# Kernel optimization log

Hardware: AMD Instinct MI355X
Metric: run time of the kernel (lower is better)

Reference implementation:

```python
import jax, jax.numpy as jnp
import numpy as np


def _operators_3_to_2(x2d, A, norm):
    # x2d: [b, d, n, n], A: [b, n, n]. Returns the 20 basis tensors, each [b, d, n, n].
    t = lambda a: a.transpose(0, 1, 3, 2)
    shape = x2d.shape
    op1 = jnp.einsum('bdij,bij,bik->bdjk', x2d, A, A) / norm
    op2 = jnp.einsum('bdij,bij,bjk->bdik', x2d, A, A) / norm
    op3 = jnp.einsum('bdij,bik,bjk->bdij', x2d, A, A) / norm
    op4 = jnp.broadcast_to(jnp.einsum('bdij,bij->bdi', x2d, A)[..., None], shape) / norm
    op5 = jnp.broadcast_to(jnp.einsum('bdij,bij->bdj', x2d, A)[..., None], shape) / norm
    op6 = jnp.einsum('bdij,bik->bdjk', x2d, A) / norm
    # NOTE: source has ops7 = [op6, op6.transpose] (bug: op7 computed but unused) -- replicated faithfully.
    op8 = jnp.einsum('bdij,bik->bdij', x2d, A) / norm
    op9 = jnp.einsum('bdij,bjk->bdij', x2d, A) / norm
    op10 = jnp.broadcast_to(x2d.sum(3, keepdims=True), shape) / norm
    op11 = jnp.broadcast_to(x2d.sum(2, keepdims=True), shape) / norm
    return [op1, t(op1), op2, t(op2), op3,
            op4, t(op4), op5, t(op5),
            op6, t(op6), op6, t(op6),
            op8, op9,
            op10, t(op10), op11, t(op11),
            x2d]


def _forward(x, edge_weight, coeffs1, bias1, coeffs2, bias2, edge_index, batch, n):
    f = x.shape[-1]
    b = x.shape[0] // n
    # to_2d_tensor: [b*n, f] -> [b, 2f, n, n]
    x2 = x.reshape(b, n, f).transpose(0, 2, 1)  # [b, f, n]
    x_2d = jnp.concatenate([
        jnp.broadcast_to(x2[:, :, :, None], (b, f, n, n)),
        jnp.broadcast_to(x2[:, :, None, :], (b, f, n, n)),
    ], axis=1)
    # to_dense_adj: scatter-add edge weights into per-graph dense [b, n, n]
    g = batch[edge_index[0]]
    r = edge_index[0] - g * n
    c = edge_index[1] - g * n
    A = jnp.zeros((b, n, n), x.dtype).at[g, r, c].add(edge_weight)
    norm = jnp.asarray(n, x.dtype)  # normalization=True default
    for li, (coeffs, bias) in enumerate([(coeffs1, bias1), (coeffs2, bias2)]):
        ops_out = jnp.stack(_operators_3_to_2(x_2d, A, norm), axis=2)  # [b, d, 20, n, n]
        x_2d = jnp.einsum('der,bdrij->beij', coeffs, ops_out) + bias
        if li == 0:
            x_2d = jax.nn.sigmoid(x_2d)
    return x_2d.mean(axis=(1, 2, 3))  # [b]


def setup_inputs() -> dict:
    key = jax.random.key(0)
    kx, kg, ks, kd, kw, kc1, kc2 = jax.random.split(key, 7)
    b, n, deg, f, h = 4, 128, 16, 32, 32
    d_in, d_out = 2 * f, 2 * h  # layer doubles channels; hidden layer is d_out -> d_out
    E = b * n * deg
    x = jax.random.normal(kx, (b * n, f), dtype=jnp.float32)
    g = jax.random.randint(kg, (E,), 0, b)
    src = jax.random.randint(ks, (E,), 0, n)
    dst = jax.random.randint(kd, (E,), 0, n)
    edge_index = jnp.stack([g * n + src, g * n + dst]).astype(jnp.int32)
    edge_weight = jax.random.uniform(kw, (E,), dtype=jnp.float32)
    batch = (jnp.arange(b * n) // n).astype(jnp.int32)
    scale1 = np.sqrt(2.0) / (d_in + d_out)
    scale2 = np.sqrt(2.0) / (d_out + d_out)
    coeffs1 = jax.random.normal(kc1, (d_in, d_out, 20), dtype=jnp.float32) * scale1
    coeffs2 = jax.random.normal(kc2, (d_out, d_out, 20), dtype=jnp.float32) * scale2
    bias1 = jnp.zeros((1, d_out, 1, 1), dtype=jnp.float32)
    bias2 = jnp.zeros((1, d_out, 1, 1), dtype=jnp.float32)
    return {"x": x, "edge_weight": edge_weight, "coeffs1": coeffs1, "bias1": bias1,
            "coeffs2": coeffs2, "bias2": bias2, "edge_index": edge_index,
            "batch": batch, "n": n}


def reference(x, edge_weight, coeffs1, bias1, coeffs2, bias2, edge_index, batch, n):
    return _forward(x, edge_weight, coeffs1, bias1, coeffs2, bias2, edge_index, batch, n)
```

## Files before the change

kernel.cpp:

```cpp
#include <hip/hip_runtime.h>
#include <stdint.h>

typedef unsigned short u16;
using short8 = __attribute__((ext_vector_type(8))) short;
using f32x4  = __attribute__((ext_vector_type(4))) float;

#define NB 4
#define NN 128
#define NF 32
#define ND 64

#define OFF_A     0u
#define OFF_ACC   262144u
#define OFF_AAT   262400u
#define OFF_RA    524544u
#define OFF_W     526592u
#define OFF_RM    1116416u
#define OFF_CM    1247488u
#define OFF_RX    1378560u
#define OFF_CX    1509632u
#define OFF_BF    1640960u
#define OFF_ATB   1641472u
#define OFF_WB    1772544u
#define OFF_X2    1936384u
#define OFF_XC    10324992u
#define OFF_CA    10357760u
#define OFF_UA    18713600u
#define OFF_UB    27102208u
#define OFF_UC    35490816u
#define OFF_UD    43879424u
#define OFF_YACC  52268032u

__device__ __forceinline__ float b2f(u16 v){
  union { uint32_t u; float f; } x; x.u = ((uint32_t)v) << 16; return x.f;
}
__device__ __forceinline__ u16 f2b(float f){
  union { uint32_t u; float f2; } x; x.f2 = f;
  uint32_t u = x.u;
  return (u16)((u + 0x7FFFu + ((u >> 16) & 1u)) >> 16);
}

#define MFMA16(a,b,c) __builtin_amdgcn_mfma_f32_16x16x32_bf16((a),(b),(c),0,0,0)

__device__ __constant__ signed char dR1[18] = {0,9,1,10,2,3,4,13,14,19,5,7,15,18,6,8,16,17};
__device__ __constant__ signed char dR2[18] = {-1,11,-1,12,-1,-1,-1,-1,-1,-1,-1,-1,-1,-1,-1,-1,-1,-1};

__global__ void k_setup(const int* __restrict__ ei, const int* __restrict__ bat,
                        const void* __restrict__ ews, float* __restrict__ A, int E,
                        const void* __restrict__ xs, u16* __restrict__ xc,
                        const void* __restrict__ c1s, const void* __restrict__ c2s,
                        const void* __restrict__ b1s, const void* __restrict__ b2s,
                        float* __restrict__ W, u16* __restrict__ Wb,
                        float* __restrict__ bfv)
{
  __shared__ int flg;
  const u16* x16 = (const u16*)xs;
  if (threadIdx.x == 0) flg = 0;
  __syncthreads();
  int hit = 0;
  for (int k = threadIdx.x; k < 1024; k += 256){
    u16 u = x16[k];
    if (((u >> 7) & 0xFF) >= 0x90) hit = 1;
  }
  if (hit) flg = 1;
  __syncthreads();
  const int isf = flg;

  const int bx = blockIdx.x;
  if (bx < 32){
    if (bx == 0 && threadIdx.x < 128){
      int tt = threadIdx.x;
      const void* bsrc = (tt < 64) ? b1s : b2s;
      int idx = tt & 63;
      bfv[tt] = isf ? ((const float*)bsrc)[idx] : b2f(((const u16*)bsrc)[idx]);
    }
    for (int t = bx*256 + threadIdx.x; t < E; t += 32*256){
      int s = ei[t], dnode = ei[E + t];
      int g = bat[s];
      int r = s - g*NN, c = dnode - g*NN;
      float wv = isf ? ((const float*)ews)[t] : b2f(((const u16*)ews)[t]);
      atomicAdd(&A[(g*NN + r)*NN + c], wv);
    }
  } else if (bx < 40){
    int idx8 = ((bx - 32)*256 + threadIdx.x)*8;
    if (!isf){
      *(short8*)(xc + idx8) = *(const short8*)(x16 + idx8);
    } else {
      const float* xfp = (const float*)xs;
      short8 v;
      #pragma unroll
      for (int k = 0; k < 8; k++) v[k] = (short)f2b(xfp[idx8 + k]);
      *(short8*)(xc + idx8) = v;
    }
  } else {
    int gl = (bx - 40)*256 + threadIdx.x;
    if (gl >= 2*1152*64) return;
    int L = gl / (1152*64);
    int rem = gl - L*1152*64;
    int row = rem >> 6, e = rem & 63;
    int slot = row >> 6, d = row & 63;
    const void* cr = L ? c2s : c1s;
    int base = (d*64 + e)*20;
    int i1 = base + dR1[slot];
    float v = isf ? ((const float*)cr)[i1] : b2f(((const u16*)cr)[i1]);
    if (dR2[slot] >= 0){
      int i2 = base + dR2[slot];
      v += isf ? ((const float*)cr)[i2] : b2f(((const u16*)cr)[i2]);
    }
    float scale = (slot == 9) ? 1.0f : (1.0f/128.0f);
    v *= scale;
    W[gl] = v;
    if (slot < 10)
      Wb[(((size_t)L*10 + slot)*64 + e)*64 + d] = f2b(v);
  }
}

__global__ __launch_bounds__(256) void k_prepA(const float* __restrict__ A, float* __restrict__ AAt,
                                               u16* __restrict__ ATb, float* __restrict__ rA,
                                               float* __restrict__ cA){
  const int iq = blockIdx.x, b = blockIdx.y;
  const int t = threadIdx.x;
  if (iq < 32){
    int j = t & 127, ih = t >> 7;
    int i0 = iq*4 + ih, i1 = i0 + 2;
    const float* Ab = A + b*NN*NN;
    float acc0 = 0.f, acc1 = 0.f;
    #pragma unroll 4
    for (int k = 0; k < 128; k += 4){
      float4 aj = *(const float4*)(Ab + j*128 + k);
      float4 a0 = *(const float4*)(Ab + i0*128 + k);
      float4 a1 = *(const float4*)(Ab + i1*128 + k);
      acc0 += a0.x*aj.x + a0.y*aj.y + a0.z*aj.z + a0.w*aj.w;
      acc1 += a1.x*aj.x + a1.y*aj.y + a1.z*aj.z + a1.w*aj.w;
    }
    AAt[(b*NN + i0)*NN + j] = acc0;
    AAt[(b*NN + i1)*NN + j] = acc1;
  } else {
    __shared__ float lds[128][129];
    for (int l = 0; l < 64; l++){
      int idx = l*256 + t;
      lds[idx >> 7][idx & 127] = A[b*16384 + idx];
    }
    __syncthreads();
    for (int l = 0; l < 64; l++){
      int idx = l*256 + t;
      int r = idx >> 7, c = idx & 127;
      ATb[b*16384 + idx] = f2b(lds[c][r]);
    }
    if (t < 128){
      float s = 0.f;
      for (int j = 0; j < 128; j++) s += lds[t][j];
      rA[b*NN + t] = s;
    } else {
      int c = t - 128;
      float s = 0.f;
      for (int j = 0; j < 128; j++) s += lds[j][c];
      cA[b*NN + c] = s;
    }
  }
}

#define SJ32 70
#define SJF  67
#define SXE  34

__global__ __launch_bounds__(256) void k_mixrow(const u16* __restrict__ Xs, const float* __restrict__ A,
    const float* __restrict__ AAt, const float* __restrict__ rA, const float* __restrict__ cA,
    const u16* __restrict__ xc, const u16* __restrict__ Wb,
    u16* __restrict__ Ua, u16* __restrict__ Ub, u16* __restrict__ Uc, u16* __restrict__ Ud,
    float* __restrict__ Yacc,
    float* __restrict__ RM, float* __restrict__ CM,
    float* __restrict__ RX, float* __restrict__ CXv, int first)
{
  const int b = blockIdx.y;
  const int t = threadIdx.x;

  if (blockIdx.x >= 256){
    const int d = blockIdx.x - 256;
    if (first){
      if (t < 128){
        const int i = t;
        if (d < NF){
          float xv = b2f(xc[(b*NN + i)*NF + d]);
          RM[(b*64 + d)*128 + i] = xv * rA[b*NN + i];
          RX[(b*64 + d)*128 + i] = 128.f * xv;
        } else {
          const u16* xcb = xc + b*NN*NF + (d - NF);
          const float* Ar = A + b*16384 + i*128;
          float sm = 0.f, sx = 0.f;
          for (int j = 0; j < 128; j++){
            float xj = b2f(xcb[j*NF]);
            sm += Ar[j]*xj; sx += xj;
          }
          RM[(b*64 + d)*128 + i] = sm;
          RX[(b*64 + d)*128 + i] = sx;
        }
      } else {
        const int j = t - 128;
        if (d < NF){
          const u16* xcb = xc + b*NN*NF + d;
          const float* Ac = A + b*16384 + j;
          float sm = 0.f, sx = 0.f;
          for (int i = 0; i < 128; i++){
            float xi = b2f(xcb[i*NF]);
            sm += Ac[i*128]*xi; sx += xi;
          }
          CM[(b*64 + d)*128 + j] = sm;
          CXv[(b*64 + d)*128 + j] = sx;
        } else {
          float xv = b2f(xc[(b*NN + j)*NF + (d - NF)]);
          CM[(b*64 + d)*128 + j] = xv * cA[b*NN + j];
          CXv[(b*64 + d)*128 + j] = 128.f * xv;
        }
      }
      return;
    }
    const u16* Xd = Xs + ((size_t)(b*ND + d) << 14);
    const float* Ab = A + b*NN*NN;
    float sm = 0.f, sx = 0.f;
    if (t < 128){
      const int i = t;
      #pragma unroll 2
      for (int j8 = 0; j8 < 16; j8++){
        short8 xv = *(const short8*)(Xd + i*128 + j8*8);
        float4 a0 = *(const float4*)(Ab + i*128 + j8*8);
        float4 a1 = *(const float4*)(Ab + i*128 + j8*8 + 4);
        float x0 = b2f((u16)xv[0]), x1 = b2f((u16)xv[1]), x2 = b2f((u16)xv[2]), x3 = b2f((u16)xv[3]);
        float x4 = b2f((u16)xv[4]), x5 = b2f((u16)xv[5]), x6 = b2f((u16)xv[6]), x7 = b2f((u16)xv[7]);
        sx += x0+x1+x2+x3+x4+x5+x6+x7;
        sm += x0*a0.x + x1*a0.y + x2*a0.z + x3*a0.w
            + x4*a1.x + x5*a1.y + x6*a1.z + x7*a1.w;
      }
      RM[(b*64 + d)*128 + i] = sm;
      RX[(b*64 + d)*128 + i] = sx;
    } else {
      const int j = t - 128;
      for (int i = 0; i < 128; i++){
        float xv = b2f(Xd[i*128 + j]);
        sx += xv;
        sm += xv * Ab[i*128 + j];
      }
      CM[(b*64 + d)*128 + j] = sm;
      CXv[(b*64 + d)*128 + j] = sx;
    }
    return;
  }

  const int w = t >> 6, lane = t & 63;
  const int col = lane & 15, quad = lane >> 4;
  const int ij0 = blockIdx.x*64;

  __shared__ uint32_t lsb[4][32*SJ32];
  __shared__ float lsf[64*SJF];

  short8 wa[10][2];
  #pragma unroll
  for (int s = 0; s < 10; s++){
    const u16* wp = Wb + (size_t)((s*64 + w*16 + col)*64 + quad*8);
    wa[s][0] = *(const short8*)wp;
    wa[s][1] = *(const short8*)(wp + 32);
  }
  float a_s[4], t_s[4], rjv[4];
  #pragma unroll
  for (int sj = 0; sj < 4; sj++){
    int ij = ij0 + sj*16 + col;
    a_s[sj] = A[b*16384 + ij];
    t_s[sj] = AAt[b*16384 + ij];
    rjv[sj] = rA[b*128 + (ij & 127)];
  }
  const float riv = rA[b*128 + (ij0 >> 7)];

  uint32_t* ldsX = &lsb[0][0];
  {
    const int ep = t >> 3;
    const int s8 = (t & 7)*8;
    if (first){
      const int i = ij0 >> 7;
      const int j0 = (ij0 & 127) + s8;
      if (ep < 16){
        uint32_t p = *(const uint32_t*)(xc + (b*NN + i)*NF + 2*ep);
        #pragma unroll
        for (int k = 0; k < 8; k++) ldsX[(s8 + k)*SXE + ep] = p;
      } else {
        const int d0 = 2*ep - 32;
        #pragma unroll
        for (int k = 0; k < 8; k++)
          ldsX[(s8 + k)*SXE + ep] = *(const uint32_t*)(xc + (b*NN + j0 + k)*NF + d0);
      }
    } else {
      const u16* xp = Xs + ((size_t)(b*ND + 2*ep) << 14) + ij0 + s8;
      short8 r0 = *(const short8*)xp;
      short8 r1 = *(const short8*)(xp + 16384);
      #pragma unroll
      for (int k = 0; k < 8; k++)
        ldsX[(s8 + k)*SXE + ep] = ((uint32_t)(u16)r0[k]) | (((uint32_t)(u16)r1[k]) << 16);
    }
  }
  __syncthreads();
  short8 xb[4][2];
  #pragma unroll
  for (int sj = 0; sj < 4; sj++){
    #pragma unroll
    for (int h = 0; h < 2; h++){
      const uint32_t* p = &ldsX[(sj*16 + col)*SXE + quad*4 + h*16];
      uint2 u0 = *(const uint2*)p;
      uint2 u1 = *(const uint2*)(p + 2);
      union { uint32_t u[4]; short8 s; } cv;
      cv.u[0] = u0.x; cv.u[1] = u0.y; cv.u[2] = u1.x; cv.u[3] = u1.y;
      xb[sj][h] = cv.s;
    }
  }
  __syncthreads();

  #pragma unroll
  for (int g = 0; g < 5; g++){
    const int s0_tab[5]  = {0, 2, 4, 5, 6};
    const int nsl_tab[5] = {2, 2, 1, 1, 4};
    const int s0 = s0_tab[g], nsl = nsl_tab[g];
    #pragma unroll
    for (int sj = 0; sj < 4; sj++){
      f32x4 acc[4];
      #pragma unroll
      for (int s = 0; s < 4; s++) acc[s] = (f32x4){0.f,0.f,0.f,0.f};
      #pragma unroll
      for (int s = 0; s < 4; s++){
        if (s >= nsl) break;
        acc[s] = MFMA16(wa[s0+s][0], xb[sj][0], acc[s]);
        acc[s] = MFMA16(wa[s0+s][1], xb[sj][1], acc[s]);
      }
      if (g < 4){
        float v[4];
        #pragma unroll
        for (int r = 0; r < 4; r++){
          if (g == 2 || g == 3) v[r] = acc[0][r]*a_s[sj];
          else                  v[r] = acc[0][r]*a_s[sj] + acc[1][r];
        }
        uint32_t p0 = (uint32_t)f2b(v[0]) | ((uint32_t)f2b(v[1]) << 16);
        uint32_t p1 = (uint32_t)f2b(v[2]) | ((uint32_t)f2b(v[3]) << 16);
        int ep = w*8 + quad*2;
        lsb[g][ep*SJ32 + sj*16 + col] = p0;
        lsb[g][(ep + 1)*SJ32 + sj*16 + col] = p1;
      } else {
        #pragma unroll
        for (int r = 0; r < 4; r++){
          float v = acc[0][r]*t_s[sj] + acc[1][r]*riv + acc[2][r]*rjv[sj] + acc[3][r];
          lsf[(w*16 + quad*4 + r)*SJF + sj*16 + col] = v;
        }
      }
    }
  }
  __syncthreads();

  const int eo = t >> 2, seg = t & 3;
  const int ep = eo >> 1, sh = (eo & 1)*16;
  #pragma unroll
  for (int g = 0; g < 4; g++){
    const uint32_t* lp = &lsb[g][ep*SJ32 + seg*16];
    short8 v0, v1;
    #pragma unroll
    for (int k = 0; k < 8; k++){
      v0[k] = (short)((lp[k]   >> sh) & 0xffffu);
      v1[k] = (short)((lp[8+k] >> sh) & 0xffffu);
    }
    u16* U = (g==0)?Ua:(g==1)?Ub:(g==2)?Uc:Ud;
    u16* dst = U + ((size_t)(b*64 + eo) << 14) + ij0 + seg*16;
    *(short8*)dst = v0;
    *(short8*)(dst + 8) = v1;
  }
  {
    const float* fp = &lsf[eo*SJF + seg*16];
    float* dst = Yacc + ((size_t)(b*64 + eo) << 14) + ij0 + seg*16;
    #pragma unroll
    for (int q = 0; q < 4; q++)
      *(float4*)(dst + q*4) = make_float4(fp[q*4], fp[q*4+1], fp[q*4+2], fp[q*4+3]);
  }
}

#define SLT 68
#define SST 136

__global__ __launch_bounds__(512) void k_tne(const u16* __restrict__ ATb,
    const u16* __restrict__ Ua, const u16* __restrict__ Ub,
    const u16* __restrict__ Uc, const u16* __restrict__ Ud,
    const float* __restrict__ Yacc, const float* __restrict__ W,
    const float* __restrict__ RM, const float* __restrict__ CM,
    const float* __restrict__ RX, const float* __restrict__ CXv,
    const float* __restrict__ bias, u16* __restrict__ Xout, float* __restrict__ acc4,
    unsigned int* __restrict__ cnt, const u16* __restrict__ x16, void* __restrict__ outp,
    int last)
{
  const int be = blockIdx.x;
  const int b = be >> 6, e = be & 63;
  const int t = threadIdx.x, wave = t >> 6, lane = t & 63;
  const int col = lane & 15, quad = lane >> 4;
  const int m0 = (wave >> 2)*64;
  const int n0 = (wave & 3)*32;

  __shared__ uint32_t uls[128*SLT];
  __shared__ uint32_t ubl[128*SLT];
  __shared__ float radd[128], cadd[128];
  __shared__ float red[8];
  __shared__ int flg, lastblk;

  if (t == 0){ flg = 0; lastblk = 0; }

  const u16* ua = Ua + ((size_t)be << 14);
  const u16* ub = Ub + ((size_t)be << 14);

  if (t < 128){
    int i = t; float s = 0.f;
    for (int d = 0; d < ND; d++){
      int v = (b*ND + d)*NN + i;
      s += W[(640 + d)*64 + e]*RM[v] + W[(704 + d)*64 + e]*CM[v]
         + W[(768 + d)*64 + e]*RX[v] + W[(832 + d)*64 + e]*CXv[v];
    }
    radd[i] = s;
  } else if (t < 256){
    int j = t - 128; float s = 0.f;
    for (int d = 0; d < ND; d++){
      int v = (b*ND + d)*NN + j;
      s += W[(896 + d)*64 + e]*RM[v] + W[(960 + d)*64 + e]*CM[v]
         + W[(1024 + d)*64 + e]*RX[v] + W[(1088 + d)*64 + e]*CXv[v];
    }
    cadd[j] = s;
  } else if (t < 384){
    const int tt = t - 256;
    const int kp = tt >> 1, p = tt & 1;
    #pragma unroll
    for (int it = 0; it < 8; it++){
      int mo = it*2 + p;
      short8 r0 = *(const short8*)(ua + (2*kp)*128 + mo*8);
      short8 r1 = *(const short8*)(ua + (2*kp + 1)*128 + mo*8);
      #pragma unroll
      for (int x = 0; x < 8; x++)
        uls[(mo*8 + x)*SLT + kp] = ((uint32_t)(u16)r0[x]) | (((uint32_t)(u16)r1[x]) << 16);
    }
  } else {
    const int tt = t - 384;
    const int kp = tt >> 1, p = tt & 1;
    #pragma unroll
    for (int it = 0; it < 8; it++){
      int no = it*2 + p;
      short8 r0 = *(const short8*)(ub + (2*kp)*128 + no*8);
      short8 r1 = *(const short8*)(ub + (2*kp + 1)*128 + no*8);
      #pragma unroll
      for (int x = 0; x < 8; x++)
        ubl[(no*8 + x)*SLT + kp] = ((uint32_t)(u16)r0[x]) | (((uint32_t)(u16)r1[x]) << 16);
    }
  }
  __syncthreads();

  f32x4 acc[4][2];
  #pragma unroll
  for (int mt = 0; mt < 4; mt++)
    #pragma unroll
    for (int nt = 0; nt < 2; nt++)
      acc[mt][nt] = (f32x4){0.f,0.f,0.f,0.f};

  const u16* at = ATb + ((size_t)b << 14);
  short8 at_n[4][2];
  #pragma unroll
  for (int kq = 0; kq < 4; kq++){
    int k0 = kq*32 + quad*8;
    at_n[kq][0] = *(const short8*)(at + (n0 + col)*128 + k0);
    at_n[kq][1] = *(const short8*)(at + (n0 + 16 + col)*128 + k0);
  }

  #pragma unroll
  for (int kq = 0; kq < 4; kq++){
    int kd = kq*16 + quad*4;
    #pragma unroll
    for (int mt = 0; mt < 4; mt++){
      short8 af = *(const short8*)&uls[(m0 + mt*16 + col)*SLT + kd];
      acc[mt][0] = MFMA16(af, at_n[kq][0], acc[mt][0]);
      acc[mt][1] = MFMA16(af, at_n[kq][1], acc[mt][1]);
    }
  }
  #pragma unroll
  for (int kq = 0; kq < 4; kq++){
    int k0 = kq*32 + quad*8, kd = kq*16 + quad*4;
    short8 bf0 = *(const short8*)&ubl[(n0 + col)*SLT + kd];
    short8 bf1 = *(const short8*)&ubl[(n0 + 16 + col)*SLT + kd];
    #pragma unroll
    for (int mt = 0; mt < 4; mt++){
      short8 af = *(const short8*)(at + (m0 + mt*16 + col)*128 + k0);
      acc[mt][0] = MFMA16(af, bf0, acc[mt][0]);
      acc[mt][1] = MFMA16(af, bf1, acc[mt][1]);
    }
  }
  {
    const u16* uc = Uc + ((size_t)be << 14);
    #pragma unroll
    for (int kq = 0; kq < 4; kq++){
      int k0 = kq*32 + quad*8;
      #pragma unroll
      for (int mt = 0; mt < 4; mt++){
        short8 af = *(const short8*)(uc + (m0 + mt*16 + col)*128 + k0);
        acc[mt][0] = MFMA16(af, at_n[kq][0], acc[mt][0]);
        acc[mt][1] = MFMA16(af, at_n[kq][1], acc[mt][1]);
      }
    }
  }
  {
    const u16* ud = Ud + ((size_t)be << 14);
    #pragma unroll
    for (int kq = 0; kq < 4; kq++){
      int k0 = kq*32 + quad*8;
      short8 bf0 = *(const short8*)(ud + (n0 + col)*128 + k0);
      short8 bf1 = *(const short8*)(ud + (n0 + 16 + col)*128 + k0);
      #pragma unroll
      for (int mt = 0; mt < 4; mt++){
        short8 af = *(const short8*)(at + (m0 + mt*16 + col)*128 + k0);
        acc[mt][0] = MFMA16(af, bf0, acc[mt][0]);
        acc[mt][1] = MFMA16(af, bf1, acc[mt][1]);
      }
    }
  }
  __syncthreads();

  uint32_t* stg = uls;
  const float bv = bias[e];
  const float* Y = Yacc + ((size_t)be << 14);
  if (!last){
    const int chalf = (n0 >> 6)*68 + (n0 & 32);
    #pragma unroll
    for (int mt = 0; mt < 4; mt++)
      #pragma unroll
      for (int nt = 0; nt < 2; nt++)
        #pragma unroll
        for (int rp = 0; rp < 2; rp++){
          uint32_t p = 0;
          #pragma unroll
          for (int h = 0; h < 2; h++){
            int r = rp*2 + h;
            int row = m0 + mt*16 + quad*4 + r;
            int cn = n0 + nt*16 + col;
            float v = acc[mt][nt][r] + Y[row*128 + cn] + radd[row] + cadd[cn] + bv;
            v = 1.f/(1.f + __expf(-v));
            p |= ((uint32_t)f2b(v)) << (16*h);
          }
          int ipair = ((m0 + mt*16 + quad*4) >> 1) + rp;
          stg[ipair*SST + chalf + nt*16 + col] = p;
        }
    __syncthreads();
    const int u = t & 255, half = t >> 8;
    const uint32_t* lp = &stg[(u >> 2)*SST + half*68 + (u & 1)*32];
    const int sh = ((u >> 1) & 1)*16;
    u16* dst = Xout + ((size_t)be << 14) + (size_t)(u >> 1)*128 + half*64 + (u & 1)*32;
    #pragma unroll
    for (int q2 = 0; q2 < 4; q2++){
      short8 v;
      #pragma unroll
      for (int k = 0; k < 8; k++) v[k] = (short)((lp[q2*8 + k] >> sh) & 0xffffu);
      *(short8*)(dst + q2*8) = v;
    }
  } else {
    float loc = 0.f;
    #pragma unroll
    for (int mt = 0; mt < 4; mt++)
      #pragma unroll
      for (int nt = 0; nt < 2; nt++)
        #pragma unroll
        for (int r = 0; r < 4; r++){
          int row = m0 + mt*16 + quad*4 + r;
          int cn = n0 + nt*16 + col;
          loc += acc[mt][nt][r] + Y[row*128 + cn] + radd[row] + cadd[cn] + bv;
        }
    for (int off = 32; off > 0; off >>= 1) loc += __shfl_down(loc, off, 64);
    if (lane == 0) red[wave] = loc;
    __syncthreads();
    if (t == 0){
      float s = 0.f;
      #pragma unroll
      for (int wv = 0; wv < 8; wv++) s += red[wv];
      atomicAdd(&acc4[b], s);
      __threadfence();
      unsigned int old = atomicAdd(cnt, 1u);
      if (old == 255u) lastblk = 1;
    }
    __syncthreads();
    if (lastblk){
      if (((x16[t] >> 7) & 0xFF) >= 0x90) flg = 1;
      __syncthreads();
      if (t < NB){
        float v = atomicAdd(&acc4[t], 0.f) * (1.0f/1048576.0f);
        if (flg) ((float*)outp)[t] = v;
        else     ((u16*)outp)[t] = f2b(v);
      }
    }
  }
}

extern "C" void kernel_launch(void* const* d_in, const int* in_sizes, int n_in,
                              void* d_out, int out_size, void* d_ws, size_t ws_size,
                              hipStream_t stream)
{
  const void* x   = d_in[0];
  const void* ew  = d_in[1];
  const void* c1  = d_in[2];
  const void* b1  = d_in[3];
  const void* c2  = d_in[4];
  const void* b2  = d_in[5];
  const int* ei  = (const int*)d_in[6];
  const int* bat = (const int*)d_in[7];
  const int E = in_sizes[1];

  char* wsb = (char*)d_ws;
  float* A    = (float*)(wsb + OFF_A);
  float* acc4 = (float*)(wsb + OFF_ACC);
  unsigned int* cnt = (unsigned int*)(wsb + OFF_ACC + 32);
  float* AAt  = (float*)(wsb + OFF_AAT);
  float* rA   = (float*)(wsb + OFF_RA);
  float* W    = (float*)(wsb + OFF_W);
  float* RM   = (float*)(wsb + OFF_RM);
  float* CM   = (float*)(wsb + OFF_CM);
  float* RX   = (float*)(wsb + OFF_RX);
  float* CXv  = (float*)(wsb + OFF_CX);
  float* bfv  = (float*)(wsb + OFF_BF);
  u16* ATb = (u16*)(wsb + OFF_ATB);
  u16* Wb  = (u16*)(wsb + OFF_WB);
  u16* X2  = (u16*)(wsb + OFF_X2);
  u16* xc  = (u16*)(wsb + OFF_XC);
  float* cA = (float*)(wsb + OFF_CA);
  u16* Ua  = (u16*)(wsb + OFF_UA);
  u16* Ub  = (u16*)(wsb + OFF_UB);
  u16* Uc  = (u16*)(wsb + OFF_UC);
  u16* Ud  = (u16*)(wsb + OFF_UD);
  float* Yacc = (float*)(wsb + OFF_YACC);

  hipMemsetAsync(wsb, 0, OFF_AAT, stream);

  k_setup<<<dim3(616), dim3(256), 0, stream>>>(ei, bat, ew, A, E, x, xc,
                                               c1, c2, b1, b2, W, Wb, bfv);
  k_prepA<<<dim3(33, NB), dim3(256), 0, stream>>>(A, AAt, ATb, rA, cA);

  for (int L = 0; L < 2; L++){
    const float* Wl = W + (size_t)L*1152*64;
    const u16*  Wbl = Wb + (size_t)L*10*64*64;
    k_mixrow<<<dim3(320, NB), dim3(256), 0, stream>>>(X2, A, AAt, rA, cA, xc, Wbl,
                                                      Ua, Ub, Uc, Ud, Yacc, RM, CM, RX, CXv,
                                                      L == 0 ? 1 : 0);
    k_tne<<<dim3(256), dim3(512), 0, stream>>>(ATb, Ua, Ub, Uc, Ud, Yacc, Wl,
                                               RM, CM, RX, CXv, bfv + L*64, X2, acc4,
                                               cnt, (const u16*)x, d_out, L);
  }
}
```

Before: 199.1 us.

## Fuse layer-2 row/column reductions into layer-1 epilogue and remap blocks to XCDs

The row/column sums (plain and A-weighted) of the layer-1 sigmoid output are now accumulated in the k_tne epilogue through shuffles and shared-memory atomics, then written to new RM2/CM2/RX2/CX2 buffers. Layer 2's k_mixrow can then skip its extra 64 reduction blocks per batch, so it no longer re-reads X2 and A from global memory. k_tne also remaps block IDs so that each XCD works on a single batch, which is meant to improve L2 locality. In exchange the epilogue does more work: it reloads A, runs shuffle reductions and issues LDS atomics. The sums are taken from bf16-rounded values, which should match what the removed pass read from X2.

```diff
diff --git a/kernel.cpp b/kernel.cpp
--- a/kernel.cpp
+++ b/kernel.cpp
@@ -25,6 +25,10 @@
 #define OFF_X2    1936384u
 #define OFF_XC    10324992u
 #define OFF_CA    10357760u
+#define OFF_RM2   10485760u
+#define OFF_CM2   10616832u
+#define OFF_RX2   10747904u
+#define OFF_CX2   10878976u
 #define OFF_UA    18713600u
 #define OFF_UB    27102208u
 #define OFF_UC    35490816u
@@ -177,71 +181,40 @@
 
   if (blockIdx.x >= 256){
     const int d = blockIdx.x - 256;
-    if (first){
-      if (t < 128){
-        const int i = t;
-        if (d < NF){
-          float xv = b2f(xc[(b*NN + i)*NF + d]);
-          RM[(b*64 + d)*128 + i] = xv * rA[b*NN + i];
-          RX[(b*64 + d)*128 + i] = 128.f * xv;
-        } else {
-          const u16* xcb = xc + b*NN*NF + (d - NF);
-          const float* Ar = A + b*16384 + i*128;
-          float sm = 0.f, sx = 0.f;
-          for (int j = 0; j < 128; j++){
-            float xj = b2f(xcb[j*NF]);
-            sm += Ar[j]*xj; sx += xj;
-          }
-          RM[(b*64 + d)*128 + i] = sm;
-          RX[(b*64 + d)*128 + i] = sx;
-        }
-      } else {
-        const int j = t - 128;
-        if (d < NF){
-          const u16* xcb = xc + b*NN*NF + d;
-          const float* Ac = A + b*16384 + j;
-          float sm = 0.f, sx = 0.f;
-          for (int i = 0; i < 128; i++){
-            float xi = b2f(xcb[i*NF]);
-            sm += Ac[i*128]*xi; sx += xi;
-          }
-          CM[(b*64 + d)*128 + j] = sm;
-          CXv[(b*64 + d)*128 + j] = sx;
-        } else {
-          float xv = b2f(xc[(b*NN + j)*NF + (d - NF)]);
-          CM[(b*64 + d)*128 + j] = xv * cA[b*NN + j];
-          CXv[(b*64 + d)*128 + j] = 128.f * xv;
-        }
-      }
-      return;
-    }
-    const u16* Xd = Xs + ((size_t)(b*ND + d) << 14);
-    const float* Ab = A + b*NN*NN;
-    float sm = 0.f, sx = 0.f;
     if (t < 128){
       const int i = t;
-      #pragma unroll 2
-      for (int j8 = 0; j8 < 16; j8++){
-        short8 xv = *(const short8*)(Xd + i*128 + j8*8);
-        float4 a0 = *(const float4*)(Ab + i*128 + j8*8);
-        float4 a1 = *(const float4*)(Ab + i*128 + j8*8 + 4);
-        float x0 = b2f((u16)xv[0]), x1 = b2f((u16)xv[1]), x2 = b2f((u16)xv[2]), x3 = b2f((u16)xv[3]);
-        float x4 = b2f((u16)xv[4]), x5 = b2f((u16)xv[5]), x6 = b2f((u16)xv[6]), x7 = b2f((u16)xv[7]);
-        sx += x0+x1+x2+x3+x4+x5+x6+x7;
-        sm += x0*a0.x + x1*a0.y + x2*a0.z + x3*a0.w
-            + x4*a1.x + x5*a1.y + x6*a1.z + x7*a1.w;
-      }
-      RM[(b*64 + d)*128 + i] = sm;
-      RX[(b*64 + d)*128 + i] = sx;
+      if (d < NF){
+        float xv = b2f(xc[(b*NN + i)*NF + d]);
+        RM[(b*64 + d)*128 + i] = xv * rA[b*NN + i];
+        RX[(b*64 + d)*128 + i] = 128.f * xv;
+      } else {
+        const u16* xcb = xc + b*NN*NF + (d - NF);
+        const float* Ar = A + b*16384 + i*128;
+        float sm = 0.f, sx = 0.f;
+        for (int j = 0; j < 128; j++){
+          float xj = b2f(xcb[j*NF]);
+          sm += Ar[j]*xj; sx += xj;
+        }
+        RM[(b*64 + d)*128 + i] = sm;
+        RX[(b*64 + d)*128 + i] = sx;
+      }
     } else {
       const int j = t - 128;
-      for (int i = 0; i < 128; i++){
-        float xv = b2f(Xd[i*128 + j]);
-        sx += xv;
-        sm += xv * Ab[i*128 + j];
-      }
-      CM[(b*64 + d)*128 + j] = sm;
-      CXv[(b*64 + d)*128 + j] = sx;
+      if (d < NF){
+        const u16* xcb = xc + b*NN*NF + d;
+        const float* Ac = A + b*16384 + j;
+        float sm = 0.f, sx = 0.f;
+        for (int i = 0; i < 128; i++){
+          float xi = b2f(xcb[i*NF]);
+          sm += Ac[i*128]*xi; sx += xi;
+        }
+        CM[(b*64 + d)*128 + j] = sm;
+        CXv[(b*64 + d)*128 + j] = sx;
+      } else {
+        float xv = b2f(xc[(b*NN + j)*NF + (d - NF)]);
+        CM[(b*64 + d)*128 + j] = xv * cA[b*NN + j];
+        CXv[(b*64 + d)*128 + j] = 128.f * xv;
+      }
     }
     return;
   }
@@ -383,14 +356,20 @@
     const u16* __restrict__ Ua, const u16* __restrict__ Ub,
     const u16* __restrict__ Uc, const u16* __restrict__ Ud,
     const float* __restrict__ Yacc, const float* __restrict__ W,
+    const float* __restrict__ Afull,
     const float* __restrict__ RM, const float* __restrict__ CM,
     const float* __restrict__ RX, const float* __restrict__ CXv,
+    float* __restrict__ RMo, float* __restrict__ CMo,
+    float* __restrict__ RXo, float* __restrict__ CXo,
     const float* __restrict__ bias, u16* __restrict__ Xout, float* __restrict__ acc4,
     unsigned int* __restrict__ cnt, const u16* __restrict__ x16, void* __restrict__ outp,
     int last)
 {
-  const int be = blockIdx.x;
-  const int b = be >> 6, e = be & 63;
+  const int bid = blockIdx.x;
+  const int xcd = bid & 7, slot = bid >> 3;
+  const int b = xcd >> 1;
+  const int e = (xcd & 1)*32 + slot;
+  const int be = b*64 + e;
   const int t = threadIdx.x, wave = t >> 6, lane = t & 63;
   const int col = lane & 15, quad = lane >> 4;
   const int m0 = (wave >> 2)*64;
@@ -399,10 +378,12 @@
   __shared__ uint32_t uls[128*SLT];
   __shared__ uint32_t ubl[128*SLT];
   __shared__ float radd[128], cadd[128];
+  __shared__ float rsM[128], rsX[128], csM[128], csX[128];
   __shared__ float red[8];
   __shared__ int flg, lastblk;
 
   if (t == 0){ flg = 0; lastblk = 0; }
+  if (t < 128){ rsM[t] = 0.f; rsX[t] = 0.f; csM[t] = 0.f; csX[t] = 0.f; }
 
   const u16* ua = Ua + ((size_t)be << 14);
   const u16* ub = Ub + ((size_t)be << 14);
@@ -523,25 +504,61 @@
   const float* Y = Yacc + ((size_t)be << 14);
   if (!last){
     const int chalf = (n0 >> 6)*68 + (n0 & 32);
-    #pragma unroll
-    for (int mt = 0; mt < 4; mt++)
-      #pragma unroll
-      for (int nt = 0; nt < 2; nt++)
-        #pragma unroll
-        for (int rp = 0; rp < 2; rp++){
-          uint32_t p = 0;
-          #pragma unroll
-          for (int h = 0; h < 2; h++){
-            int r = rp*2 + h;
-            int row = m0 + mt*16 + quad*4 + r;
-            int cn = n0 + nt*16 + col;
-            float v = acc[mt][nt][r] + Y[row*128 + cn] + radd[row] + cadd[cn] + bv;
-            v = 1.f/(1.f + __expf(-v));
-            p |= ((uint32_t)f2b(v)) << (16*h);
-          }
-          int ipair = ((m0 + mt*16 + quad*4) >> 1) + rp;
-          stg[ipair*SST + chalf + nt*16 + col] = p;
+    const float* Ab = Afull + b*16384;
+    float colM[2] = {0.f, 0.f}, colX[2] = {0.f, 0.f};
+    #pragma unroll
+    for (int mt = 0; mt < 4; mt++){
+      uint32_t pk[2][2];
+      #pragma unroll
+      for (int r = 0; r < 4; r++){
+        int row = m0 + mt*16 + quad*4 + r;
+        float vv[2], aa[2];
+        #pragma unroll
+        for (int nt = 0; nt < 2; nt++){
+          int cn = n0 + nt*16 + col;
+          float v = acc[mt][nt][r] + Y[row*128 + cn] + radd[row] + cadd[cn] + bv;
+          v = 1.f/(1.f + __expf(-v));
+          u16 vb = f2b(v);
+          if (r & 1) pk[r>>1][nt] |= ((uint32_t)vb) << 16;
+          else       pk[r>>1][nt]  = (uint32_t)vb;
+          vv[nt] = b2f(vb);
+          aa[nt] = Ab[row*128 + cn];
         }
+        float pr  = vv[0] + vv[1];
+        float prM = vv[0]*aa[0] + vv[1]*aa[1];
+        #pragma unroll
+        for (int m = 1; m < 16; m <<= 1){
+          pr  += __shfl_xor(pr,  m, 64);
+          prM += __shfl_xor(prM, m, 64);
+        }
+        if (col == 0){ atomicAdd(&rsX[row], pr); atomicAdd(&rsM[row], prM); }
+        colX[0] += vv[0]; colX[1] += vv[1];
+        colM[0] += vv[0]*aa[0]; colM[1] += vv[1]*aa[1];
+      }
+      #pragma unroll
+      for (int rp = 0; rp < 2; rp++){
+        int ipair = ((m0 + mt*16 + quad*4) >> 1) + rp;
+        #pragma unroll
+        for (int nt = 0; nt < 2; nt++)
+          stg[ipair*SST + chalf + nt*16 + col] = pk[rp][nt];
+      }
+    }
+    #pragma unroll
+    for (int m = 16; m < 64; m <<= 1){
+      #pragma unroll
+      for (int nt = 0; nt < 2; nt++){
+        colX[nt] += __shfl_xor(colX[nt], m, 64);
+        colM[nt] += __shfl_xor(colM[nt], m, 64);
+      }
+    }
+    if (quad == 0){
+      #pragma unroll
+      for (int nt = 0; nt < 2; nt++){
+        int cn = n0 + nt*16 + col;
+        atomicAdd(&csX[cn], colX[nt]);
+        atomicAdd(&csM[cn], colM[nt]);
+      }
+    }
     __syncthreads();
     const int u = t & 255, half = t >> 8;
     const uint32_t* lp = &stg[(u >> 2)*SST + half*68 + (u & 1)*32];
@@ -553,6 +570,14 @@
       #pragma unroll
       for (int k = 0; k < 8; k++) v[k] = (short)((lp[q2*8 + k] >> sh) & 0xffffu);
       *(short8*)(dst + q2*8) = v;
+    }
+    if (t < 128){
+      int o = (b*64 + e)*128 + t;
+      RMo[o] = rsM[t]; RXo[o] = rsX[t];
+    } else if (t < 256){
+      int j = t - 128;
+      int o = (b*64 + e)*128 + j;
+      CMo[o] = csM[j]; CXo[o] = csX[j];
     }
   } else {
     float loc = 0.f;
@@ -616,6 +641,10 @@
   float* CM   = (float*)(wsb + OFF_CM);
   float* RX   = (float*)(wsb + OFF_RX);
   float* CXv  = (float*)(wsb + OFF_CX);
+  float* RM2  = (float*)(wsb + OFF_RM2);
+  float* CM2  = (float*)(wsb + OFF_CM2);
+  float* RX2  = (float*)(wsb + OFF_RX2);
+  float* CX2  = (float*)(wsb + OFF_CX2);
   float* bfv  = (float*)(wsb + OFF_BF);
   u16* ATb = (u16*)(wsb + OFF_ATB);
   u16* Wb  = (u16*)(wsb + OFF_WB);
@@ -637,11 +666,17 @@
   for (int L = 0; L < 2; L++){
     const float* Wl = W + (size_t)L*1152*64;
     const u16*  Wbl = Wb + (size_t)L*10*64*64;
-    k_mixrow<<<dim3(320, NB), dim3(256), 0, stream>>>(X2, A, AAt, rA, cA, xc, Wbl,
-                                                      Ua, Ub, Uc, Ud, Yacc, RM, CM, RX, CXv,
-                                                      L == 0 ? 1 : 0);
-    k_tne<<<dim3(256), dim3(512), 0, stream>>>(ATb, Ua, Ub, Uc, Ud, Yacc, Wl,
-                                               RM, CM, RX, CXv, bfv + L*64, X2, acc4,
+    const float* RMi = (L == 0) ? RM : RM2;
+    const float* CMi = (L == 0) ? CM : CM2;
+    const float* RXi = (L == 0) ? RX : RX2;
+    const float* CXi = (L == 0) ? CXv : CX2;
+    k_mixrow<<<dim3(L == 0 ? 320 : 256, NB), dim3(256), 0, stream>>>(
+        X2, A, AAt, rA, cA, xc, Wbl,
+        Ua, Ub, Uc, Ud, Yacc, RM, CM, RX, CXv, L == 0 ? 1 : 0);
+    k_tne<<<dim3(256), dim3(512), 0, stream>>>(ATb, Ua, Ub, Uc, Ud, Yacc, Wl, A,
+                                               RMi, CMi, RXi, CXi,
+                                               RM2, CM2, RX2, CX2,
+                                               bfv + L*64, X2, acc4,
                                                cnt, (const u16*)x, d_out, L);
   }
 }
```

Result: slower. 242.5 us (+21.8%).

## Split k_tne output tile into quadrants across four times more blocks

Applied to the files above, without the earlier changes.

Each k_tne block now handles a 64x64 quadrant of the 128x128 output per (batch, channel) instead of the full tile. This gives 1024 blocks of 256 threads rather than 256 blocks of 512, which should fill the GPU better and cut the LDS each block needs. The row and column bias reductions are split across thread pairs over halves of the d loop and then combined in shared memory. In exchange, the A^T operand and the U transposes are loaded redundantly across quadrant blocks, and the completion counter and final flag check are adjusted for the new block count.

```diff
diff --git a/kernel.cpp b/kernel.cpp
--- a/kernel.cpp
+++ b/kernel.cpp
@@ -377,9 +377,9 @@
 }
 
 #define SLT 68
-#define SST 136
-
-__global__ __launch_bounds__(512) void k_tne(const u16* __restrict__ ATb,
+#define SSTQ 68
+
+__global__ __launch_bounds__(256) void k_tne(const u16* __restrict__ ATb,
     const u16* __restrict__ Ua, const u16* __restrict__ Ub,
     const u16* __restrict__ Uc, const u16* __restrict__ Ud,
     const float* __restrict__ Yacc, const float* __restrict__ W,
@@ -389,17 +389,19 @@
     unsigned int* __restrict__ cnt, const u16* __restrict__ x16, void* __restrict__ outp,
     int last)
 {
-  const int be = blockIdx.x;
+  const int bid = blockIdx.x;
+  const int be = bid >> 2;
   const int b = be >> 6, e = be & 63;
+  const int mh = (bid >> 1) & 1, nh = bid & 1;
   const int t = threadIdx.x, wave = t >> 6, lane = t & 63;
   const int col = lane & 15, quad = lane >> 4;
-  const int m0 = (wave >> 2)*64;
-  const int n0 = (wave & 3)*32;
-
-  __shared__ uint32_t uls[128*SLT];
-  __shared__ uint32_t ubl[128*SLT];
-  __shared__ float radd[128], cadd[128];
-  __shared__ float red[8];
+  const int m0 = mh*64 + (wave >> 1)*32;
+  const int n0 = nh*64 + (wave & 1)*32;
+
+  __shared__ uint32_t uls[64*SLT];
+  __shared__ uint32_t ubl[64*SLT];
+  __shared__ float radd[64], cadd[64], prt[256];
+  __shared__ float red[4];
   __shared__ int flg, lastblk;
 
   if (t == 0){ flg = 0; lastblk = 0; }
@@ -407,52 +409,59 @@
   const u16* ua = Ua + ((size_t)be << 14);
   const u16* ub = Ub + ((size_t)be << 14);
 
-  if (t < 128){
-    int i = t; float s = 0.f;
-    for (int d = 0; d < ND; d++){
-      int v = (b*ND + d)*NN + i;
-      s += W[(640 + d)*64 + e]*RM[v] + W[(704 + d)*64 + e]*CM[v]
-         + W[(768 + d)*64 + e]*RX[v] + W[(832 + d)*64 + e]*CXv[v];
-    }
-    radd[i] = s;
-  } else if (t < 256){
-    int j = t - 128; float s = 0.f;
-    for (int d = 0; d < ND; d++){
-      int v = (b*ND + d)*NN + j;
-      s += W[(896 + d)*64 + e]*RM[v] + W[(960 + d)*64 + e]*CM[v]
-         + W[(1024 + d)*64 + e]*RX[v] + W[(1088 + d)*64 + e]*CXv[v];
-    }
-    cadd[j] = s;
-  } else if (t < 384){
-    const int tt = t - 256;
-    const int kp = tt >> 1, p = tt & 1;
-    #pragma unroll
-    for (int it = 0; it < 8; it++){
-      int mo = it*2 + p;
-      short8 r0 = *(const short8*)(ua + (2*kp)*128 + mo*8);
-      short8 r1 = *(const short8*)(ua + (2*kp + 1)*128 + mo*8);
-      #pragma unroll
-      for (int x = 0; x < 8; x++)
-        uls[(mo*8 + x)*SLT + kp] = ((uint32_t)(u16)r0[x]) | (((uint32_t)(u16)r1[x]) << 16);
-    }
-  } else {
-    const int tt = t - 384;
-    const int kp = tt >> 1, p = tt & 1;
-    #pragma unroll
-    for (int it = 0; it < 8; it++){
-      int no = it*2 + p;
-      short8 r0 = *(const short8*)(ub + (2*kp)*128 + no*8);
-      short8 r1 = *(const short8*)(ub + (2*kp + 1)*128 + no*8);
-      #pragma unroll
-      for (int x = 0; x < 8; x++)
-        ubl[(no*8 + x)*SLT + kp] = ((uint32_t)(u16)r0[x]) | (((uint32_t)(u16)r1[x]) << 16);
-    }
+  {
+    const int tt = t & 127, kp = tt >> 1, p = tt & 1;
+    if (t < 128){
+      #pragma unroll
+      for (int it = 0; it < 4; it++){
+        int mo = mh*8 + it*2 + p;
+        short8 r0 = *(const short8*)(ua + (2*kp)*128 + mo*8);
+        short8 r1 = *(const short8*)(ua + (2*kp + 1)*128 + mo*8);
+        int lr = (mo - mh*8)*8;
+        #pragma unroll
+        for (int x = 0; x < 8; x++)
+          uls[(lr + x)*SLT + kp] = ((uint32_t)(u16)r0[x]) | (((uint32_t)(u16)r1[x]) << 16);
+      }
+    } else {
+      #pragma unroll
+      for (int it = 0; it < 4; it++){
+        int no = nh*8 + it*2 + p;
+        short8 r0 = *(const short8*)(ub + (2*kp)*128 + no*8);
+        short8 r1 = *(const short8*)(ub + (2*kp + 1)*128 + no*8);
+        int lr = (no - nh*8)*8;
+        #pragma unroll
+        for (int x = 0; x < 8; x++)
+          ubl[(lr + x)*SLT + kp] = ((uint32_t)(u16)r0[x]) | (((uint32_t)(u16)r1[x]) << 16);
+      }
+    }
+  }
+  {
+    const int idx = (t >> 1) & 63, dh = t & 1;
+    float s = 0.f;
+    if (t < 128){
+      int i = mh*64 + idx;
+      for (int d = dh*32; d < dh*32 + 32; d++){
+        int v = (b*ND + d)*NN + i;
+        s += W[(640 + d)*64 + e]*RM[v] + W[(704 + d)*64 + e]*CM[v]
+           + W[(768 + d)*64 + e]*RX[v] + W[(832 + d)*64 + e]*CXv[v];
+      }
+    } else {
+      int j = nh*64 + idx;
+      for (int d = dh*32; d < dh*32 + 32; d++){
+        int v = (b*ND + d)*NN + j;
+        s += W[(896 + d)*64 + e]*RM[v] + W[(960 + d)*64 + e]*CM[v]
+           + W[(1024 + d)*64 + e]*RX[v] + W[(1088 + d)*64 + e]*CXv[v];
+      }
+    }
+    prt[t] = s;
   }
   __syncthreads();
-
-  f32x4 acc[4][2];
-  #pragma unroll
-  for (int mt = 0; mt < 4; mt++)
+  if (t < 64)       radd[t] = prt[2*t] + prt[2*t + 1];
+  else if (t < 128) cadd[t - 64] = prt[128 + 2*(t - 64)] + prt[128 + 2*(t - 64) + 1];
+
+  f32x4 acc[2][2];
+  #pragma unroll
+  for (int mt = 0; mt < 2; mt++)
     #pragma unroll
     for (int nt = 0; nt < 2; nt++)
       acc[mt][nt] = (f32x4){0.f,0.f,0.f,0.f};
@@ -470,8 +479,8 @@
   for (int kq = 0; kq < 4; kq++){
     int kd = kq*16 + quad*4;
     #pragma unroll
-    for (int mt = 0; mt < 4; mt++){
-      short8 af = *(const short8*)&uls[(m0 + mt*16 + col)*SLT + kd];
+    for (int mt = 0; mt < 2; mt++){
+      short8 af = *(const short8*)&uls[((wave >> 1)*32 + mt*16 + col)*SLT + kd];
       acc[mt][0] = MFMA16(af, at_n[kq][0], acc[mt][0]);
       acc[mt][1] = MFMA16(af, at_n[kq][1], acc[mt][1]);
     }
@@ -479,10 +488,10 @@
   #pragma unroll
   for (int kq = 0; kq < 4; kq++){
     int k0 = kq*32 + quad*8, kd = kq*16 + quad*4;
-    short8 bf0 = *(const short8*)&ubl[(n0 + col)*SLT + kd];
-    short8 bf1 = *(const short8*)&ubl[(n0 + 16 + col)*SLT + kd];
-    #pragma unroll
-    for (int mt = 0; mt < 4; mt++){
+    short8 bf0 = *(const short8*)&ubl[((wave & 1)*32 + col)*SLT + kd];
+    short8 bf1 = *(const short8*)&ubl[((wave & 1)*32 + 16 + col)*SLT + kd];
+    #pragma unroll
+    for (int mt = 0; mt < 2; mt++){
       short8 af = *(const short8*)(at + (m0 + mt*16 + col)*128 + k0);
       acc[mt][0] = MFMA16(af, bf0, acc[mt][0]);
       acc[mt][1] = MFMA16(af, bf1, acc[mt][1]);
@@ -494,7 +503,7 @@
     for (int kq = 0; kq < 4; kq++){
       int k0 = kq*32 + quad*8;
       #pragma unroll
-      for (int mt = 0; mt < 4; mt++){
+      for (int mt = 0; mt < 2; mt++){
         short8 af = *(const short8*)(uc + (m0 + mt*16 + col)*128 + k0);
         acc[mt][0] = MFMA16(af, at_n[kq][0], acc[mt][0]);
         acc[mt][1] = MFMA16(af, at_n[kq][1], acc[mt][1]);
@@ -509,7 +518,7 @@
       short8 bf0 = *(const short8*)(ud + (n0 + col)*128 + k0);
       short8 bf1 = *(const short8*)(ud + (n0 + 16 + col)*128 + k0);
       #pragma unroll
-      for (int mt = 0; mt < 4; mt++){
+      for (int mt = 0; mt < 2; mt++){
         short8 af = *(const short8*)(at + (m0 + mt*16 + col)*128 + k0);
         acc[mt][0] = MFMA16(af, bf0, acc[mt][0]);
         acc[mt][1] = MFMA16(af, bf1, acc[mt][1]);
@@ -522,9 +531,8 @@
   const float bv = bias[e];
   const float* Y = Yacc + ((size_t)be << 14);
   if (!last){
-    const int chalf = (n0 >> 6)*68 + (n0 & 32);
-    #pragma unroll
-    for (int mt = 0; mt < 4; mt++)
+    #pragma unroll
+    for (int mt = 0; mt < 2; mt++)
       #pragma unroll
       for (int nt = 0; nt < 2; nt++)
         #pragma unroll
@@ -533,22 +541,23 @@
           #pragma unroll
           for (int h = 0; h < 2; h++){
             int r = rp*2 + h;
-            int row = m0 + mt*16 + quad*4 + r;
-            int cn = n0 + nt*16 + col;
-            float v = acc[mt][nt][r] + Y[row*128 + cn] + radd[row] + cadd[cn] + bv;
+            int lrow = (wave >> 1)*32 + mt*16 + quad*4 + r;
+            int lcol = (wave & 1)*32 + nt*16 + col;
+            float v = acc[mt][nt][r] + Y[(mh*64 + lrow)*128 + nh*64 + lcol]
+                    + radd[lrow] + cadd[lcol] + bv;
             v = 1.f/(1.f + __expf(-v));
             p |= ((uint32_t)f2b(v)) << (16*h);
           }
-          int ipair = ((m0 + mt*16 + quad*4) >> 1) + rp;
-          stg[ipair*SST + chalf + nt*16 + col] = p;
+          int ipair = (wave >> 1)*16 + mt*8 + quad*2 + rp;
+          stg[ipair*SSTQ + (wave & 1)*32 + nt*16 + col] = p;
         }
     __syncthreads();
-    const int u = t & 255, half = t >> 8;
-    const uint32_t* lp = &stg[(u >> 2)*SST + half*68 + (u & 1)*32];
-    const int sh = ((u >> 1) & 1)*16;
-    u16* dst = Xout + ((size_t)be << 14) + (size_t)(u >> 1)*128 + half*64 + (u & 1)*32;
-    #pragma unroll
-    for (int q2 = 0; q2 < 4; q2++){
+    const int lr = t >> 2, seg = t & 3;
+    const uint32_t* lp = &stg[(lr >> 1)*SSTQ + seg*16];
+    const int sh = (lr & 1)*16;
+    u16* dst = Xout + ((size_t)be << 14) + (size_t)(mh*64 + lr)*128 + nh*64 + seg*16;
+    #pragma unroll
+    for (int q2 = 0; q2 < 2; q2++){
       short8 v;
       #pragma unroll
       for (int k = 0; k < 8; k++) v[k] = (short)((lp[q2*8 + k] >> sh) & 0xffffu);
@@ -557,30 +566,30 @@
   } else {
     float loc = 0.f;
     #pragma unroll
-    for (int mt = 0; mt < 4; mt++)
+    for (int mt = 0; mt < 2; mt++)
       #pragma unroll
       for (int nt = 0; nt < 2; nt++)
         #pragma unroll
         for (int r = 0; r < 4; r++){
-          int row = m0 + mt*16 + quad*4 + r;
-          int cn = n0 + nt*16 + col;
-          loc += acc[mt][nt][r] + Y[row*128 + cn] + radd[row] + cadd[cn] + bv;
+          int lrow = (wave >> 1)*32 + mt*16 + quad*4 + r;
+          int lcol = (wave & 1)*32 + nt*16 + col;
+          loc += acc[mt][nt][r] + Y[(mh*64 + lrow)*128 + nh*64 + lcol]
+               + radd[lrow] + cadd[lcol] + bv;
         }
     for (int off = 32; off > 0; off >>= 1) loc += __shfl_down(loc, off, 64);
     if (lane == 0) red[wave] = loc;
     __syncthreads();
     if (t == 0){
-      float s = 0.f;
-      #pragma unroll
-      for (int wv = 0; wv < 8; wv++) s += red[wv];
+      float s = red[0] + red[1] + red[2] + red[3];
       atomicAdd(&acc4[b], s);
       __threadfence();
       unsigned int old = atomicAdd(cnt, 1u);
-      if (old == 255u) lastblk = 1;
+      if (old == 1023u) lastblk = 1;
     }
     __syncthreads();
     if (lastblk){
-      if (((x16[t] >> 7) & 0xFF) >= 0x90) flg = 1;
+      for (int k = t; k < 512; k += 256)
+        if (((x16[k] >> 7) & 0xFF) >= 0x90) flg = 1;
       __syncthreads();
       if (t < NB){
         float v = atomicAdd(&acc4[t], 0.f) * (1.0f/1048576.0f);
@@ -640,8 +649,8 @@
     k_mixrow<<<dim3(320, NB), dim3(256), 0, stream>>>(X2, A, AAt, rA, cA, xc, Wbl,
                                                       Ua, Ub, Uc, Ud, Yacc, RM, CM, RX, CXv,
                                                       L == 0 ? 1 : 0);
-    k_tne<<<dim3(256), dim3(512), 0, stream>>>(ATb, Ua, Ub, Uc, Ud, Yacc, Wl,
-                                               RM, CM, RX, CXv, bfv + L*64, X2, acc4,
-                                               cnt, (const u16*)x, d_out, L);
+    k_tne<<<dim3(1024), dim3(256), 0, stream>>>(ATb, Ua, Ub, Uc, Ud, Yacc, Wl,
+                                                RM, CM, RX, CXv, bfv + L*64, X2, acc4,
+                                                cnt, (const u16*)x, d_out, L);
   }
 }
```

New measurement: 261.3 us. 1.31x slower.
